# Optimization experiments

Measured on AMD Instinct MI355X. Metric: run time of the kernel, lower is better.

The kernel has to match this reference:

```python
import jax, jax.numpy as jnp
import numpy as np

B, C_IN, C_OUT, H, W = 16, 192, 192, 128, 128
K_EXPERTS, LATENT_DIM = 8, 64


def setup_inputs() -> dict:
    key = jax.random.key(0)
    ks = jax.random.split(key, 6)
    s = lambda fan: np.float32(1.0 / np.sqrt(fan))
    return {
        "x": jax.random.normal(ks[0], (B, C_IN, H, W), jnp.float32),
        "latent": jax.random.normal(ks[1], (B, LATENT_DIM), jnp.float32),
        # DyConv2d: K expert 3x3 kernels + biases, attention FC from latent
        "expert_w": jax.random.normal(ks[2], (K_EXPERTS, C_OUT, C_IN, 3, 3), jnp.float32) * s(C_IN * 9),
        "expert_b": jnp.zeros((K_EXPERTS, C_OUT), jnp.float32),
        "attn_w": jax.random.normal(ks[3], (K_EXPERTS, LATENT_DIM), jnp.float32) * s(LATENT_DIM),
        "attn_b": jnp.zeros((K_EXPERTS,), jnp.float32),
        # static conv2 (3x3) weights
        "conv2_w": jax.random.normal(ks[4], (C_OUT, C_OUT, 3, 3), jnp.float32) * s(C_OUT * 9),
        "conv2_b": jnp.zeros((C_OUT,), jnp.float32),
    }


def _conv3x3(x, w, b):
    # x: [N,C,H,W], w: [O,I,3,3] -> [N,O,H,W]
    y = jax.lax.conv_general_dilated(
        x, w, window_strides=(1, 1), padding=((1, 1), (1, 1)),
        dimension_numbers=("NCHW", "OIHW", "NCHW"))
    return y + b[None, :, None, None]


def reference(x, latent, expert_w, expert_b, attn_w, attn_b, conv2_w, conv2_b):
    identity = x  # stride=1, in_ch==out_ch -> adaptor is None
    # ---- DyConv2d: latent -> expert attention -> per-sample kernel ----
    attn = jax.nn.softmax(latent @ attn_w.T + attn_b, axis=-1)        # [B,K]
    w_dyn = jnp.einsum("bk,koihw->boihw", attn, expert_w)            # [B,O,I,3,3]
    b_dyn = attn @ expert_b                                          # [B,O]
    # per-sample conv, vectorized over batch
    out = jax.vmap(lambda xi, wi, bi: _conv3x3(xi[None], wi, bi)[0])(x, w_dyn, b_dyn)
    out = jax.nn.silu(out)
    # ---- static conv3x3 ----
    out = _conv3x3(out, conv2_w, conv2_b)
    out = jax.nn.silu(out)
    return out + identity
```

## Files before the change

### kernel.cpp

```cpp
#include <hip/hip_runtime.h>
#include <stdint.h>
#include <stddef.h>

typedef __bf16 bf16;
typedef bf16 bf16x8 __attribute__((ext_vector_type(8)));
typedef bf16 bf16x4 __attribute__((ext_vector_type(4)));
typedef float f32x4 __attribute__((ext_vector_type(4)));

#define B_   16
#define CI   192
#define CO   192
#define H_   128
#define W_   128
#define KE   8
#define LD   64
#define KTOT 1728
#define HP   130
#define HPHP (HP*HP)
#define NPX  (H_*W_)
#define NT   54

__device__ __forceinline__ void gll16(const void* g, void* l) {
  __builtin_amdgcn_global_load_lds(
      (const __attribute__((address_space(1))) unsigned int*)g,
      (__attribute__((address_space(3))) unsigned int*)l, 16, 0, 0);
}

__device__ __forceinline__ float silu_f(float x) {
  return x / (1.f + __expf(-x));
}

__global__ void k_attn(const float* __restrict__ latent, const float* __restrict__ attn_w,
                       const float* __restrict__ attn_b, float* __restrict__ attn) {
  int t = threadIdx.x;
  int b = t >> 3, k = t & 7;
  float s = attn_b[k];
  for (int d = 0; d < LD; ++d) s += latent[b*LD + d] * attn_w[k*LD + d];
  float m = s;
  for (int off = 4; off; off >>= 1) m = fmaxf(m, __shfl_xor(m, off, 8));
  float e = __expf(s - m);
  float sum = e;
  for (int off = 4; off; off >>= 1) sum += __shfl_xor(sum, off, 8);
  attn[t] = e / sum;
}

__global__ void k_bdyn(const float* __restrict__ attn, const float* __restrict__ expert_b,
                       float* __restrict__ bdyn) {
  int j = blockIdx.x * 256 + threadIdx.x;
  if (j >= B_ * CO) return;
  int b = j / CO, o = j - b * CO;
  float s = 0.f;
  #pragma unroll
  for (int e = 0; e < KE; ++e) s += attn[b*KE + e] * expert_b[e*CO + o];
  bdyn[j] = s;
}

__global__ void k_wdyn(const float* __restrict__ expert_w, const float* __restrict__ attn,
                       bf16* __restrict__ w_re) {
  int o = blockIdx.x;
  int chunk = o >> 4, row = o & 15, c = (row >> 1) & 3;
  __shared__ float ew[KE][KTOT];
  __shared__ float al[B_][KE];
  for (int e = 0; e < KE; ++e)
    for (int j = threadIdx.x; j < KTOT; j += 256)
      ew[e][j] = expert_w[((size_t)e*CO + o)*KTOT + j];
  if (threadIdx.x < B_*KE) al[threadIdx.x >> 3][threadIdx.x & 7] = attn[threadIdx.x];
  __syncthreads();
  for (int idx = threadIdx.x; idx < B_*KTOT; idx += 256) {
    int b = idx / KTOT, k = idx - b*KTOT;
    int kt = k >> 5, ks = (k >> 3) & 3, j = k & 7;
    int r = kt / 18, t2 = kt - r*18;
    int ibb = t2 / 3, s = t2 - ibb*3;
    int i = ibb*32 + ks*8 + j;
    float acc = 0.f;
    #pragma unroll
    for (int e = 0; e < KE; ++e) acc += al[b][e] * ew[e][i*9 + r*3 + s];
    int slot = row*4 + (ks ^ c);
    w_re[((((size_t)b*NT + kt)*12 + chunk)*64 + slot)*8 + j] = (bf16)acc;
  }
}

__global__ void k_w2re(const float* __restrict__ conv2_w, bf16* __restrict__ w2_re) {
  int o = blockIdx.x;
  int chunk = o >> 4, row = o & 15, c = (row >> 1) & 3;
  __shared__ float cw[KTOT];
  for (int j = threadIdx.x; j < KTOT; j += 256) cw[j] = conv2_w[(size_t)o*KTOT + j];
  __syncthreads();
  for (int k = threadIdx.x; k < KTOT; k += 256) {
    int kt = k >> 5, ks = (k >> 3) & 3, j = k & 7;
    int r = kt / 18, t2 = kt - r*18;
    int ibb = t2 / 3, s = t2 - ibb*3;
    int i = ibb*32 + ks*8 + j;
    int slot = row*4 + (ks ^ c);
    w2_re[(((size_t)kt*12 + chunk)*64 + slot)*8 + j] = (bf16)cw[i*9 + r*3 + s];
  }
}

__global__ void k_xpack(const float* __restrict__ x, bf16* __restrict__ xpack) {
  int h2 = blockIdx.x, ib = blockIdx.y, b = blockIdx.z;
  size_t rowbase = (((size_t)b*24 + ib)*HP + h2)*HP;
  int t = threadIdx.x;
  if (h2 == 0 || h2 == HP-1) {
    uint4 z = make_uint4(0,0,0,0);
    for (int w = t; w < HP; w += 128) *(uint4*)(xpack + (rowbase + w)*8) = z;
    return;
  }
  __shared__ float tt[8][128];
  int h = h2 - 1;
  #pragma unroll
  for (int ii = 0; ii < 8; ++ii)
    tt[ii][t] = x[(((size_t)b*CI + ib*8 + ii)*H_ + h)*W_ + t];
  __syncthreads();
  bf16x8 v;
  #pragma unroll
  for (int ii = 0; ii < 8; ++ii) v[ii] = (bf16)tt[ii][t];
  *(bf16x8*)(xpack + (rowbase + t + 1)*8) = v;
  if (t == 0) {
    uint4 z = make_uint4(0,0,0,0);
    *(uint4*)(xpack + rowbase*8) = z;
    *(uint4*)(xpack + (rowbase + HP-1)*8) = z;
  }
}

__global__ void k_midborder(bf16* __restrict__ midpack) {
  int bi = blockIdx.x;
  size_t base = (size_t)bi * HPHP;
  uint4 z = make_uint4(0,0,0,0);
  for (int j = threadIdx.x; j < 516; j += 256) {
    int h2, w2;
    if (j < 130)      { h2 = 0;       w2 = j; }
    else if (j < 260) { h2 = 129;     w2 = j - 130; }
    else if (j < 388) { h2 = j - 259; w2 = 0; }
    else              { h2 = j - 387; w2 = 129; }
    *(uint4*)(midpack + (base + (size_t)h2*HP + w2)*8) = z;
  }
}

template<int MODE>
__global__ __launch_bounds__(256, 2)
void k_conv(const bf16* __restrict__ wre, const bf16* __restrict__ inpack,
            const float* __restrict__ bias_g, const bf16* __restrict__ respack,
            bf16* __restrict__ outpack, float* __restrict__ outp) {
  const int tid  = threadIdx.x;
  const int lane = tid & 63;
  const int wv   = tid >> 6;
  const int wm   = wv >> 1;
  const int wn   = wv & 1;
  const int l15  = lane & 15, l4 = lane >> 4;

  const int bid  = blockIdx.x;
  const int n    = (bid & 7) * 128 + (bid >> 3);
  const int b    = n >> 6;
  const int tile = n & 63;
  const int p0   = tile * 256;
  const int h0   = tile * 2;

  __shared__ __align__(16) bf16 Alds[3][12*512];
  __shared__ __align__(16) bf16 Blds[2][4*2560];
  __shared__ float bias_lds[CO];

  if (tid < CO) bias_lds[tid] = (MODE == 0) ? bias_g[b*CO + tid] : bias_g[tid];

  const size_t wbase = (MODE == 0) ? ((size_t)b*CO*KTOT) : 0;

  const bf16* aS = wre + wbase + (size_t)wv*512 + lane*8;
  const bf16* bbase = inpack + (((size_t)b*24 + wv)*HPHP + (size_t)h0*HP)*8 + lane*8;
  int ibm = 0; ptrdiff_t boffEl = 0;

  auto stageA = [&](bf16* dbuf) {
    bf16* d = dbuf + wv*512;
    gll16(aS,        d);
    gll16(aS + 2048, d + 2048);
    gll16(aS + 4096, d + 4096);
    aS += 6144;
  };
  auto stageB = [&](bf16* dbuf) {
    const bf16* src = bbase + boffEl;
    bf16* d = dbuf + wv*2560;
    gll16(src,        d);
    gll16(src +  512, d +  512);
    gll16(src + 1024, d + 1024);
    gll16(src + 1536, d + 1536);
    gll16(src + 1568, d + 1568);
    if (++ibm == 6) { ibm = 0; boffEl += (ptrdiff_t)(HP - 20*HPHP)*8; }
    else boffEl += (ptrdiff_t)4*HPHP*8;
  };

  f32x4 acc[6][8];
  #pragma unroll
  for (int mf = 0; mf < 6; ++mf)
    #pragma unroll
    for (int nf = 0; nf < 8; ++nf)
      #pragma unroll
      for (int jj = 0; jj < 4; ++jj) acc[mf][nf][jj] = 0.f;

  const int sw = l15*4 + (l4 ^ ((l15 >> 1) & 3));
  const int bvb = l4*2560 + (wn*130 + l15)*8;

  stageA(Alds[0]);
  stageA(Alds[1]);
  stageB(Blds[0]);

  bf16* Bcur = (bf16*)Blds[0];
  bf16* Bnxt = (bf16*)Blds[1];

  for (int m = 0; m < 18; ++m) {
    #pragma unroll
    for (int s = 0; s < 3; ++s) {
      if (s == 2) {
        if (m == 17) asm volatile("s_waitcnt vmcnt(0)" ::: "memory");
        else         asm volatile("s_waitcnt vmcnt(8)" ::: "memory");
      } else {
        asm volatile("s_waitcnt vmcnt(3)" ::: "memory");
      }
      __builtin_amdgcn_s_barrier();

      const bf16* A = Alds[s];
      const bf16* bp = Bcur + bvb + s*8;

      bf16x8 af0 = *(const bf16x8*)(A + (wm*6 + 0)*512 + sw*8);
      bf16x8 af1 = *(const bf16x8*)(A + (wm*6 + 1)*512 + sw*8);
      bf16x8 af2 = *(const bf16x8*)(A + (wm*6 + 2)*512 + sw*8);
      bf16x8 af3 = *(const bf16x8*)(A + (wm*6 + 3)*512 + sw*8);
      bf16x8 af4 = *(const bf16x8*)(A + (wm*6 + 4)*512 + sw*8);
      bf16x8 af5 = *(const bf16x8*)(A + (wm*6 + 5)*512 + sw*8);
      bf16x8 bv0 = *(const bf16x8*)(bp);
      bf16x8 bv1 = *(const bf16x8*)(bp + 128);
      bf16x8 bv2 = *(const bf16x8*)(bp + 256);
      bf16x8 bv3 = *(const bf16x8*)(bp + 384);

      if (3*m + s + 2 < NT) stageA(Alds[(s+2)%3]);

      __builtin_amdgcn_s_barrier();
      __builtin_amdgcn_s_setprio(1);
      acc[0][0] = __builtin_amdgcn_mfma_f32_16x16x32_bf16(af0, bv0, acc[0][0], 0, 0, 0);
      acc[1][0] = __builtin_amdgcn_mfma_f32_16x16x32_bf16(af1, bv0, acc[1][0], 0, 0, 0);
      acc[2][0] = __builtin_amdgcn_mfma_f32_16x16x32_bf16(af2, bv0, acc[2][0], 0, 0, 0);
      acc[3][0] = __builtin_amdgcn_mfma_f32_16x16x32_bf16(af3, bv0, acc[3][0], 0, 0, 0);
      acc[4][0] = __builtin_amdgcn_mfma_f32_16x16x32_bf16(af4, bv0, acc[4][0], 0, 0, 0);
      acc[5][0] = __builtin_amdgcn_mfma_f32_16x16x32_bf16(af5, bv0, acc[5][0], 0, 0, 0);
      acc[0][1] = __builtin_amdgcn_mfma_f32_16x16x32_bf16(af0, bv1, acc[0][1], 0, 0, 0);
      acc[1][1] = __builtin_amdgcn_mfma_f32_16x16x32_bf16(af1, bv1, acc[1][1], 0, 0, 0);
      acc[2][1] = __builtin_amdgcn_mfma_f32_16x16x32_bf16(af2, bv1, acc[2][1], 0, 0, 0);
      acc[3][1] = __builtin_amdgcn_mfma_f32_16x16x32_bf16(af3, bv1, acc[3][1], 0, 0, 0);
      acc[4][1] = __builtin_amdgcn_mfma_f32_16x16x32_bf16(af4, bv1, acc[4][1], 0, 0, 0);
      acc[5][1] = __builtin_amdgcn_mfma_f32_16x16x32_bf16(af5, bv1, acc[5][1], 0, 0, 0);
      acc[0][2] = __builtin_amdgcn_mfma_f32_16x16x32_bf16(af0, bv2, acc[0][2], 0, 0, 0);
      acc[1][2] = __builtin_amdgcn_mfma_f32_16x16x32_bf16(af1, bv2, acc[1][2], 0, 0, 0);
      acc[2][2] = __builtin_amdgcn_mfma_f32_16x16x32_bf16(af2, bv2, acc[2][2], 0, 0, 0);
      acc[3][2] = __builtin_amdgcn_mfma_f32_16x16x32_bf16(af3, bv2, acc[3][2], 0, 0, 0);
      acc[4][2] = __builtin_amdgcn_mfma_f32_16x16x32_bf16(af4, bv2, acc[4][2], 0, 0, 0);
      acc[5][2] = __builtin_amdgcn_mfma_f32_16x16x32_bf16(af5, bv2, acc[5][2], 0, 0, 0);
      acc[0][3] = __builtin_amdgcn_mfma_f32_16x16x32_bf16(af0, bv3, acc[0][3], 0, 0, 0);
      acc[1][3] = __builtin_amdgcn_mfma_f32_16x16x32_bf16(af1, bv3, acc[1][3], 0, 0, 0);
      acc[2][3] = __builtin_amdgcn_mfma_f32_16x16x32_bf16(af2, bv3, acc[2][3], 0, 0, 0);
      acc[3][3] = __builtin_amdgcn_mfma_f32_16x16x32_bf16(af3, bv3, acc[3][3], 0, 0, 0);
      acc[4][3] = __builtin_amdgcn_mfma_f32_16x16x32_bf16(af4, bv3, acc[4][3], 0, 0, 0);
      acc[5][3] = __builtin_amdgcn_mfma_f32_16x16x32_bf16(af5, bv3, acc[5][3], 0, 0, 0);
      __builtin_amdgcn_s_setprio(0);

      bf16x8 bv4 = *(const bf16x8*)(bp + 512);
      bf16x8 bv5 = *(const bf16x8*)(bp + 640);
      bf16x8 bv6 = *(const bf16x8*)(bp + 768);
      bf16x8 bv7 = *(const bf16x8*)(bp + 896);

      if (s == 1 && m < 17) stageB(Bnxt);

      __builtin_amdgcn_s_barrier();
      __builtin_amdgcn_s_setprio(1);
      acc[0][4] = __builtin_amdgcn_mfma_f32_16x16x32_bf16(af0, bv4, acc[0][4], 0, 0, 0);
      acc[1][4] = __builtin_amdgcn_mfma_f32_16x16x32_bf16(af1, bv4, acc[1][4], 0, 0, 0);
      acc[2][4] = __builtin_amdgcn_mfma_f32_16x16x32_bf16(af2, bv4, acc[2][4], 0, 0, 0);
      acc[3][4] = __builtin_amdgcn_mfma_f32_16x16x32_bf16(af3, bv4, acc[3][4], 0, 0, 0);
      acc[4][4] = __builtin_amdgcn_mfma_f32_16x16x32_bf16(af4, bv4, acc[4][4], 0, 0, 0);
      acc[5][4] = __builtin_amdgcn_mfma_f32_16x16x32_bf16(af5, bv4, acc[5][4], 0, 0, 0);
      acc[0][5] = __builtin_amdgcn_mfma_f32_16x16x32_bf16(af0, bv5, acc[0][5], 0, 0, 0);
      acc[1][5] = __builtin_amdgcn_mfma_f32_16x16x32_bf16(af1, bv5, acc[1][5], 0, 0, 0);
      acc[2][5] = __builtin_amdgcn_mfma_f32_16x16x32_bf16(af2, bv5, acc[2][5], 0, 0, 0);
      acc[3][5] = __builtin_amdgcn_mfma_f32_16x16x32_bf16(af3, bv5, acc[3][5], 0, 0, 0);
      acc[4][5] = __builtin_amdgcn_mfma_f32_16x16x32_bf16(af4, bv5, acc[4][5], 0, 0, 0);
      acc[5][5] = __builtin_amdgcn_mfma_f32_16x16x32_bf16(af5, bv5, acc[5][5], 0, 0, 0);
      acc[0][6] = __builtin_amdgcn_mfma_f32_16x16x32_bf16(af0, bv6, acc[0][6], 0, 0, 0);
      acc[1][6] = __builtin_amdgcn_mfma_f32_16x16x32_bf16(af1, bv6, acc[1][6], 0, 0, 0);
      acc[2][6] = __builtin_amdgcn_mfma_f32_16x16x32_bf16(af2, bv6, acc[2][6], 0, 0, 0);
      acc[3][6] = __builtin_amdgcn_mfma_f32_16x16x32_bf16(af3, bv6, acc[3][6], 0, 0, 0);
      acc[4][6] = __builtin_amdgcn_mfma_f32_16x16x32_bf16(af4, bv6, acc[4][6], 0, 0, 0);
      acc[5][6] = __builtin_amdgcn_mfma_f32_16x16x32_bf16(af5, bv6, acc[5][6], 0, 0, 0);
      acc[0][7] = __builtin_amdgcn_mfma_f32_16x16x32_bf16(af0, bv7, acc[0][7], 0, 0, 0);
      acc[1][7] = __builtin_amdgcn_mfma_f32_16x16x32_bf16(af1, bv7, acc[1][7], 0, 0, 0);
      acc[2][7] = __builtin_amdgcn_mfma_f32_16x16x32_bf16(af2, bv7, acc[2][7], 0, 0, 0);
      acc[3][7] = __builtin_amdgcn_mfma_f32_16x16x32_bf16(af3, bv7, acc[3][7], 0, 0, 0);
      acc[4][7] = __builtin_amdgcn_mfma_f32_16x16x32_bf16(af4, bv7, acc[4][7], 0, 0, 0);
      acc[5][7] = __builtin_amdgcn_mfma_f32_16x16x32_bf16(af5, bv7, acc[5][7], 0, 0, 0);
      __builtin_amdgcn_s_setprio(0);
    }
    { bf16* t = Bcur; Bcur = Bnxt; Bnxt = t; }
  }

  #pragma unroll
  for (int mf = 0; mf < 6; ++mf) {
    int ob = wm*96 + mf*16 + l4*4;
    #pragma unroll
    for (int nf = 0; nf < 8; ++nf) {
      int pl = wn*128 + nf*16 + l15;
      int p  = p0 + pl;
      f32x4 v = acc[mf][nf];
      int h = p >> 7, w = p & 127;
      size_t basep = (((size_t)b*24 + (ob >> 3))*HP + (h + 1))*HP + (w + 1);
      if (MODE == 0) {
        bf16x4 pk;
        #pragma unroll
        for (int jj = 0; jj < 4; ++jj) {
          float xv = v[jj] + bias_lds[ob + jj];
          pk[jj] = (bf16)silu_f(xv);
        }
        *(bf16x4*)(outpack + basep*8 + (ob & 7)) = pk;
      } else {
        bf16x4 rr = *(const bf16x4*)(respack + basep*8 + (ob & 7));
        #pragma unroll
        for (int jj = 0; jj < 4; ++jj) {
          float xv = silu_f(v[jj] + bias_lds[ob + jj]);
          size_t idx = ((size_t)b*CO + ob + jj)*NPX + p;
          outp[idx] = xv + (float)rr[jj];
        }
      }
    }
  }
}

extern "C" void kernel_launch(void* const* d_in, const int* in_sizes, int n_in,
                              void* d_out, int out_size, void* d_ws, size_t ws_size,
                              hipStream_t stream) {
  const float* x        = (const float*)d_in[0];
  const float* latent   = (const float*)d_in[1];
  const float* expert_w = (const float*)d_in[2];
  const float* expert_b = (const float*)d_in[3];
  const float* attn_w   = (const float*)d_in[4];
  const float* attn_b   = (const float*)d_in[5];
  const float* conv2_w  = (const float*)d_in[6];
  const float* conv2_b  = (const float*)d_in[7];
  float* outp = (float*)d_out;

  char* base = (char*)d_ws;
  size_t off = 0;
  float* attn = (float*)(base + off); off += 4096;
  float* bdyn = (float*)(base + off); off += 16384;
  bf16* w_re  = (bf16*)(base + off);  off += (size_t)B_*CO*KTOT*2;
  bf16* w2_re = (bf16*)(base + off);  off += (size_t)CO*KTOT*2;
  bf16* xpack = (bf16*)(base + off);  off += (size_t)B_*24*HPHP*8*2;
  bf16* midpack = (bf16*)(base + off); off += (size_t)B_*24*HPHP*8*2;
  (void)ws_size; (void)in_sizes; (void)n_in; (void)out_size;

  k_attn<<<dim3(1), dim3(128), 0, stream>>>(latent, attn_w, attn_b, attn);
  k_bdyn<<<dim3(12), dim3(256), 0, stream>>>(attn, expert_b, bdyn);
  k_wdyn<<<dim3(CO), dim3(256), 0, stream>>>(expert_w, attn, w_re);
  k_w2re<<<dim3(CO), dim3(256), 0, stream>>>(conv2_w, w2_re);
  k_xpack<<<dim3(130, 24, 16), dim3(128), 0, stream>>>(x, xpack);
  k_midborder<<<dim3(B_*24), dim3(256), 0, stream>>>(midpack);
  k_conv<0><<<dim3(1024), dim3(256), 0, stream>>>(w_re, xpack, bdyn, xpack, midpack, outp);
  k_conv<1><<<dim3(1024), dim3(256), 0, stream>>>(w2_re, midpack, conv2_b, xpack, midpack, outp);
}
```

Before: 483.5 us.

## Load conv weight fragments directly from global into registers, dropping A LDS staging

Removes the triple-buffered LDS staging of the weight (A) operand. Each wave now reads its six weight fragments straight from global memory into registers at every k-step. The B tile pitch shrinks from 2560 to 2080 elements, and the per-substep barriers and manual vmcnt waits are collapsed into one __syncthreads per outer iteration. This cuts LDS footprint, LDS traffic and barrier count, which could also allow more resident blocks. The cost is that weight loads are issued right before the MFMAs with no prefetch, so global/L2 latency may be exposed every step. Correctness relies on __syncthreads draining the outstanding global-to-LDS B loads.

```diff
diff --git a/kernel.cpp b/kernel.cpp
--- a/kernel.cpp
+++ b/kernel.cpp
@@ -155,28 +155,17 @@
   const int p0   = tile * 256;
   const int h0   = tile * 2;
 
-  __shared__ __align__(16) bf16 Alds[3][12*512];
-  __shared__ __align__(16) bf16 Blds[2][4*2560];
+  __shared__ __align__(16) bf16 Blds[2][4*2080];
   __shared__ float bias_lds[CO];
 
-  if (tid < CO) bias_lds[tid] = (MODE == 0) ? bias_g[b*CO + tid] : bias_g[tid];
-
   const size_t wbase = (MODE == 0) ? ((size_t)b*CO*KTOT) : 0;
 
-  const bf16* aS = wre + wbase + (size_t)wv*512 + lane*8;
   const bf16* bbase = inpack + (((size_t)b*24 + wv)*HPHP + (size_t)h0*HP)*8 + lane*8;
   int ibm = 0; ptrdiff_t boffEl = 0;
 
-  auto stageA = [&](bf16* dbuf) {
-    bf16* d = dbuf + wv*512;
-    gll16(aS,        d);
-    gll16(aS + 2048, d + 2048);
-    gll16(aS + 4096, d + 4096);
-    aS += 6144;
-  };
   auto stageB = [&](bf16* dbuf) {
     const bf16* src = bbase + boffEl;
-    bf16* d = dbuf + wv*2560;
+    bf16* d = dbuf + wv*2080;
     gll16(src,        d);
     gll16(src +  512, d +  512);
     gll16(src + 1024, d + 1024);
@@ -186,6 +175,13 @@
     else boffEl += (ptrdiff_t)4*HPHP*8;
   };
 
+  stageB((bf16*)Blds[0]);
+
+  if (tid < CO) bias_lds[tid] = (MODE == 0) ? bias_g[b*CO + tid] : bias_g[tid];
+
+  const int sw = l15*4 + (l4 ^ ((l15 >> 1) & 3));
+  const bf16* aptr = wre + wbase + (size_t)(wm*6)*512 + (size_t)sw*8;
+
   f32x4 acc[6][8];
   #pragma unroll
   for (int mf = 0; mf < 6; ++mf)
@@ -194,106 +190,87 @@
       #pragma unroll
       for (int jj = 0; jj < 4; ++jj) acc[mf][nf][jj] = 0.f;
 
-  const int sw = l15*4 + (l4 ^ ((l15 >> 1) & 3));
-  const int bvb = l4*2560 + (wn*130 + l15)*8;
-
-  stageA(Alds[0]);
-  stageA(Alds[1]);
-  stageB(Blds[0]);
+  const int bvb = l4*2080 + (wn*130 + l15)*8;
 
   bf16* Bcur = (bf16*)Blds[0];
   bf16* Bnxt = (bf16*)Blds[1];
 
+  auto micro = [&](const bf16* Bc, int s, bool dostage, bf16* stagebuf) {
+    bf16x8 af0 = *(const bf16x8*)(aptr);
+    bf16x8 af1 = *(const bf16x8*)(aptr +  512);
+    bf16x8 af2 = *(const bf16x8*)(aptr + 1024);
+    bf16x8 af3 = *(const bf16x8*)(aptr + 1536);
+    bf16x8 af4 = *(const bf16x8*)(aptr + 2048);
+    bf16x8 af5 = *(const bf16x8*)(aptr + 2560);
+    aptr += 6144;
+    if (dostage) stageB(stagebuf);
+    const bf16* bp = Bc + bvb + s*8;
+    bf16x8 bv0 = *(const bf16x8*)(bp);
+    bf16x8 bv1 = *(const bf16x8*)(bp + 128);
+    bf16x8 bv2 = *(const bf16x8*)(bp + 256);
+    bf16x8 bv3 = *(const bf16x8*)(bp + 384);
+    bf16x8 bv4 = *(const bf16x8*)(bp + 512);
+    bf16x8 bv5 = *(const bf16x8*)(bp + 640);
+    bf16x8 bv6 = *(const bf16x8*)(bp + 768);
+    bf16x8 bv7 = *(const bf16x8*)(bp + 896);
+    __builtin_amdgcn_s_setprio(1);
+    acc[0][0] = __builtin_amdgcn_mfma_f32_16x16x32_bf16(af0, bv0, acc[0][0], 0, 0, 0);
+    acc[1][0] = __builtin_amdgcn_mfma_f32_16x16x32_bf16(af1, bv0, acc[1][0], 0, 0, 0);
+    acc[2][0] = __builtin_amdgcn_mfma_f32_16x16x32_bf16(af2, bv0, acc[2][0], 0, 0, 0);
+    acc[3][0] = __builtin_amdgcn_mfma_f32_16x16x32_bf16(af3, bv0, acc[3][0], 0, 0, 0);
+    acc[4][0] = __builtin_amdgcn_mfma_f32_16x16x32_bf16(af4, bv0, acc[4][0], 0, 0, 0);
+    acc[5][0] = __builtin_amdgcn_mfma_f32_16x16x32_bf16(af5, bv0, acc[5][0], 0, 0, 0);
+    acc[0][1] = __builtin_amdgcn_mfma_f32_16x16x32_bf16(af0, bv1, acc[0][1], 0, 0, 0);
+    acc[1][1] = __builtin_amdgcn_mfma_f32_16x16x32_bf16(af1, bv1, acc[1][1], 0, 0, 0);
+    acc[2][1] = __builtin_amdgcn_mfma_f32_16x16x32_bf16(af2, bv1, acc[2][1], 0, 0, 0);
+    acc[3][1] = __builtin_amdgcn_mfma_f32_16x16x32_bf16(af3, bv1, acc[3][1], 0, 0, 0);
+    acc[4][1] = __builtin_amdgcn_mfma_f32_16x16x32_bf16(af4, bv1, acc[4][1], 0, 0, 0);
+    acc[5][1] = __builtin_amdgcn_mfma_f32_16x16x32_bf16(af5, bv1, acc[5][1], 0, 0, 0);
+    acc[0][2] = __builtin_amdgcn_mfma_f32_16x16x32_bf16(af0, bv2, acc[0][2], 0, 0, 0);
+    acc[1][2] = __builtin_amdgcn_mfma_f32_16x16x32_bf16(af1, bv2, acc[1][2], 0, 0, 0);
+    acc[2][2] = __builtin_amdgcn_mfma_f32_16x16x32_bf16(af2, bv2, acc[2][2], 0, 0, 0);
+    acc[3][2] = __builtin_amdgcn_mfma_f32_16x16x32_bf16(af3, bv2, acc[3][2], 0, 0, 0);
+    acc[4][2] = __builtin_amdgcn_mfma_f32_16x16x32_bf16(af4, bv2, acc[4][2], 0, 0, 0);
+    acc[5][2] = __builtin_amdgcn_mfma_f32_16x16x32_bf16(af5, bv2, acc[5][2], 0, 0, 0);
+    acc[0][3] = __builtin_amdgcn_mfma_f32_16x16x32_bf16(af0, bv3, acc[0][3], 0, 0, 0);
+    acc[1][3] = __builtin_amdgcn_mfma_f32_16x16x32_bf16(af1, bv3, acc[1][3], 0, 0, 0);
+    acc[2][3] = __builtin_amdgcn_mfma_f32_16x16x32_bf16(af2, bv3, acc[2][3], 0, 0, 0);
+    acc[3][3] = __builtin_amdgcn_mfma_f32_16x16x32_bf16(af3, bv3, acc[3][3], 0, 0, 0);
+    acc[4][3] = __builtin_amdgcn_mfma_f32_16x16x32_bf16(af4, bv3, acc[4][3], 0, 0, 0);
+    acc[5][3] = __builtin_amdgcn_mfma_f32_16x16x32_bf16(af5, bv3, acc[5][3], 0, 0, 0);
+    acc[0][4] = __builtin_amdgcn_mfma_f32_16x16x32_bf16(af0, bv4, acc[0][4], 0, 0, 0);
+    acc[1][4] = __builtin_amdgcn_mfma_f32_16x16x32_bf16(af1, bv4, acc[1][4], 0, 0, 0);
+    acc[2][4] = __builtin_amdgcn_mfma_f32_16x16x32_bf16(af2, bv4, acc[2][4], 0, 0, 0);
+    acc[3][4] = __builtin_amdgcn_mfma_f32_16x16x32_bf16(af3, bv4, acc[3][4], 0, 0, 0);
+    acc[4][4] = __builtin_amdgcn_mfma_f32_16x16x32_bf16(af4, bv4, acc[4][4], 0, 0, 0);
+    acc[5][4] = __builtin_amdgcn_mfma_f32_16x16x32_bf16(af5, bv4, acc[5][4], 0, 0, 0);
+    acc[0][5] = __builtin_amdgcn_mfma_f32_16x16x32_bf16(af0, bv5, acc[0][5], 0, 0, 0);
+    acc[1][5] = __builtin_amdgcn_mfma_f32_16x16x32_bf16(af1, bv5, acc[1][5], 0, 0, 0);
+    acc[2][5] = __builtin_amdgcn_mfma_f32_16x16x32_bf16(af2, bv5, acc[2][5], 0, 0, 0);
+    acc[3][5] = __builtin_amdgcn_mfma_f32_16x16x32_bf16(af3, bv5, acc[3][5], 0, 0, 0);
+    acc[4][5] = __builtin_amdgcn_mfma_f32_16x16x32_bf16(af4, bv5, acc[4][5], 0, 0, 0);
+    acc[5][5] = __builtin_amdgcn_mfma_f32_16x16x32_bf16(af5, bv5, acc[5][5], 0, 0, 0);
+    acc[0][6] = __builtin_amdgcn_mfma_f32_16x16x32_bf16(af0, bv6, acc[0][6], 0, 0, 0);
+    acc[1][6] = __builtin_amdgcn_mfma_f32_16x16x32_bf16(af1, bv6, acc[1][6], 0, 0, 0);
+    acc[2][6] = __builtin_amdgcn_mfma_f32_16x16x32_bf16(af2, bv6, acc[2][6], 0, 0, 0);
+    acc[3][6] = __builtin_amdgcn_mfma_f32_16x16x32_bf16(af3, bv6, acc[3][6], 0, 0, 0);
+    acc[4][6] = __builtin_amdgcn_mfma_f32_16x16x32_bf16(af4, bv6, acc[4][6], 0, 0, 0);
+    acc[5][6] = __builtin_amdgcn_mfma_f32_16x16x32_bf16(af5, bv6, acc[5][6], 0, 0, 0);
+    acc[0][7] = __builtin_amdgcn_mfma_f32_16x16x32_bf16(af0, bv7, acc[0][7], 0, 0, 0);
+    acc[1][7] = __builtin_amdgcn_mfma_f32_16x16x32_bf16(af1, bv7, acc[1][7], 0, 0, 0);
+    acc[2][7] = __builtin_amdgcn_mfma_f32_16x16x32_bf16(af2, bv7, acc[2][7], 0, 0, 0);
+    acc[3][7] = __builtin_amdgcn_mfma_f32_16x16x32_bf16(af3, bv7, acc[3][7], 0, 0, 0);
+    acc[4][7] = __builtin_amdgcn_mfma_f32_16x16x32_bf16(af4, bv7, acc[4][7], 0, 0, 0);
+    acc[5][7] = __builtin_amdgcn_mfma_f32_16x16x32_bf16(af5, bv7, acc[5][7], 0, 0, 0);
+    __builtin_amdgcn_s_setprio(0);
+    __builtin_amdgcn_sched_barrier(0);
+  };
+
   for (int m = 0; m < 18; ++m) {
-    #pragma unroll
-    for (int s = 0; s < 3; ++s) {
-      if (s == 2) {
-        if (m == 17) asm volatile("s_waitcnt vmcnt(0)" ::: "memory");
-        else         asm volatile("s_waitcnt vmcnt(8)" ::: "memory");
-      } else {
-        asm volatile("s_waitcnt vmcnt(3)" ::: "memory");
-      }
-      __builtin_amdgcn_s_barrier();
-
-      const bf16* A = Alds[s];
-      const bf16* bp = Bcur + bvb + s*8;
-
-      bf16x8 af0 = *(const bf16x8*)(A + (wm*6 + 0)*512 + sw*8);
-      bf16x8 af1 = *(const bf16x8*)(A + (wm*6 + 1)*512 + sw*8);
-      bf16x8 af2 = *(const bf16x8*)(A + (wm*6 + 2)*512 + sw*8);
-      bf16x8 af3 = *(const bf16x8*)(A + (wm*6 + 3)*512 + sw*8);
-      bf16x8 af4 = *(const bf16x8*)(A + (wm*6 + 4)*512 + sw*8);
-      bf16x8 af5 = *(const bf16x8*)(A + (wm*6 + 5)*512 + sw*8);
-      bf16x8 bv0 = *(const bf16x8*)(bp);
-      bf16x8 bv1 = *(const bf16x8*)(bp + 128);
-      bf16x8 bv2 = *(const bf16x8*)(bp + 256);
-      bf16x8 bv3 = *(const bf16x8*)(bp + 384);
-
-      if (3*m + s + 2 < NT) stageA(Alds[(s+2)%3]);
-
-      __builtin_amdgcn_s_barrier();
-      __builtin_amdgcn_s_setprio(1);
-      acc[0][0] = __builtin_amdgcn_mfma_f32_16x16x32_bf16(af0, bv0, acc[0][0], 0, 0, 0);
-      acc[1][0] = __builtin_amdgcn_mfma_f32_16x16x32_bf16(af1, bv0, acc[1][0], 0, 0, 0);
-      acc[2][0] = __builtin_amdgcn_mfma_f32_16x16x32_bf16(af2, bv0, acc[2][0], 0, 0, 0);
-      acc[3][0] = __builtin_amdgcn_mfma_f32_16x16x32_bf16(af3, bv0, acc[3][0], 0, 0, 0);
-      acc[4][0] = __builtin_amdgcn_mfma_f32_16x16x32_bf16(af4, bv0, acc[4][0], 0, 0, 0);
-      acc[5][0] = __builtin_amdgcn_mfma_f32_16x16x32_bf16(af5, bv0, acc[5][0], 0, 0, 0);
-      acc[0][1] = __builtin_amdgcn_mfma_f32_16x16x32_bf16(af0, bv1, acc[0][1], 0, 0, 0);
-      acc[1][1] = __builtin_amdgcn_mfma_f32_16x16x32_bf16(af1, bv1, acc[1][1], 0, 0, 0);
-      acc[2][1] = __builtin_amdgcn_mfma_f32_16x16x32_bf16(af2, bv1, acc[2][1], 0, 0, 0);
-      acc[3][1] = __builtin_amdgcn_mfma_f32_16x16x32_bf16(af3, bv1, acc[3][1], 0, 0, 0);
-      acc[4][1] = __builtin_amdgcn_mfma_f32_16x16x32_bf16(af4, bv1, acc[4][1], 0, 0, 0);
-      acc[5][1] = __builtin_amdgcn_mfma_f32_16x16x32_bf16(af5, bv1, acc[5][1], 0, 0, 0);
-      acc[0][2] = __builtin_amdgcn_mfma_f32_16x16x32_bf16(af0, bv2, acc[0][2], 0, 0, 0);
-      acc[1][2] = __builtin_amdgcn_mfma_f32_16x16x32_bf16(af1, bv2, acc[1][2], 0, 0, 0);
-      acc[2][2] = __builtin_amdgcn_mfma_f32_16x16x32_bf16(af2, bv2, acc[2][2], 0, 0, 0);
-      acc[3][2] = __builtin_amdgcn_mfma_f32_16x16x32_bf16(af3, bv2, acc[3][2], 0, 0, 0);
-      acc[4][2] = __builtin_amdgcn_mfma_f32_16x16x32_bf16(af4, bv2, acc[4][2], 0, 0, 0);
-      acc[5][2] = __builtin_amdgcn_mfma_f32_16x16x32_bf16(af5, bv2, acc[5][2], 0, 0, 0);
-      acc[0][3] = __builtin_amdgcn_mfma_f32_16x16x32_bf16(af0, bv3, acc[0][3], 0, 0, 0);
-      acc[1][3] = __builtin_amdgcn_mfma_f32_16x16x32_bf16(af1, bv3, acc[1][3], 0, 0, 0);
-      acc[2][3] = __builtin_amdgcn_mfma_f32_16x16x32_bf16(af2, bv3, acc[2][3], 0, 0, 0);
-      acc[3][3] = __builtin_amdgcn_mfma_f32_16x16x32_bf16(af3, bv3, acc[3][3], 0, 0, 0);
-      acc[4][3] = __builtin_amdgcn_mfma_f32_16x16x32_bf16(af4, bv3, acc[4][3], 0, 0, 0);
-      acc[5][3] = __builtin_amdgcn_mfma_f32_16x16x32_bf16(af5, bv3, acc[5][3], 0, 0, 0);
-      __builtin_amdgcn_s_setprio(0);
-
-      bf16x8 bv4 = *(const bf16x8*)(bp + 512);
-      bf16x8 bv5 = *(const bf16x8*)(bp + 640);
-      bf16x8 bv6 = *(const bf16x8*)(bp + 768);
-      bf16x8 bv7 = *(const bf16x8*)(bp + 896);
-
-      if (s == 1 && m < 17) stageB(Bnxt);
-
-      __builtin_amdgcn_s_barrier();
-      __builtin_amdgcn_s_setprio(1);
-      acc[0][4] = __builtin_amdgcn_mfma_f32_16x16x32_bf16(af0, bv4, acc[0][4], 0, 0, 0);
-      acc[1][4] = __builtin_amdgcn_mfma_f32_16x16x32_bf16(af1, bv4, acc[1][4], 0, 0, 0);
-      acc[2][4] = __builtin_amdgcn_mfma_f32_16x16x32_bf16(af2, bv4, acc[2][4], 0, 0, 0);
-      acc[3][4] = __builtin_amdgcn_mfma_f32_16x16x32_bf16(af3, bv4, acc[3][4], 0, 0, 0);
-      acc[4][4] = __builtin_amdgcn_mfma_f32_16x16x32_bf16(af4, bv4, acc[4][4], 0, 0, 0);
-      acc[5][4] = __builtin_amdgcn_mfma_f32_16x16x32_bf16(af5, bv4, acc[5][4], 0, 0, 0);
-      acc[0][5] = __builtin_amdgcn_mfma_f32_16x16x32_bf16(af0, bv5, acc[0][5], 0, 0, 0);
-      acc[1][5] = __builtin_amdgcn_mfma_f32_16x16x32_bf16(af1, bv5, acc[1][5], 0, 0, 0);
-      acc[2][5] = __builtin_amdgcn_mfma_f32_16x16x32_bf16(af2, bv5, acc[2][5], 0, 0, 0);
-      acc[3][5] = __builtin_amdgcn_mfma_f32_16x16x32_bf16(af3, bv5, acc[3][5], 0, 0, 0);
-      acc[4][5] = __builtin_amdgcn_mfma_f32_16x16x32_bf16(af4, bv5, acc[4][5], 0, 0, 0);
-      acc[5][5] = __builtin_amdgcn_mfma_f32_16x16x32_bf16(af5, bv5, acc[5][5], 0, 0, 0);
-      acc[0][6] = __builtin_amdgcn_mfma_f32_16x16x32_bf16(af0, bv6, acc[0][6], 0, 0, 0);
-      acc[1][6] = __builtin_amdgcn_mfma_f32_16x16x32_bf16(af1, bv6, acc[1][6], 0, 0, 0);
-      acc[2][6] = __builtin_amdgcn_mfma_f32_16x16x32_bf16(af2, bv6, acc[2][6], 0, 0, 0);
-      acc[3][6] = __builtin_amdgcn_mfma_f32_16x16x32_bf16(af3, bv6, acc[3][6], 0, 0, 0);
-      acc[4][6] = __builtin_amdgcn_mfma_f32_16x16x32_bf16(af4, bv6, acc[4][6], 0, 0, 0);
-      acc[5][6] = __builtin_amdgcn_mfma_f32_16x16x32_bf16(af5, bv6, acc[5][6], 0, 0, 0);
-      acc[0][7] = __builtin_amdgcn_mfma_f32_16x16x32_bf16(af0, bv7, acc[0][7], 0, 0, 0);
-      acc[1][7] = __builtin_amdgcn_mfma_f32_16x16x32_bf16(af1, bv7, acc[1][7], 0, 0, 0);
-      acc[2][7] = __builtin_amdgcn_mfma_f32_16x16x32_bf16(af2, bv7, acc[2][7], 0, 0, 0);
-      acc[3][7] = __builtin_amdgcn_mfma_f32_16x16x32_bf16(af3, bv7, acc[3][7], 0, 0, 0);
-      acc[4][7] = __builtin_amdgcn_mfma_f32_16x16x32_bf16(af4, bv7, acc[4][7], 0, 0, 0);
-      acc[5][7] = __builtin_amdgcn_mfma_f32_16x16x32_bf16(af5, bv7, acc[5][7], 0, 0, 0);
-      __builtin_amdgcn_s_setprio(0);
-    }
+    __syncthreads();
+    micro(Bcur, 0, false, nullptr);
+    micro(Bcur, 1, false, nullptr);
+    micro(Bcur, 2, m < 17, Bnxt);
     { bf16* t = Bcur; Bcur = Bnxt; Bnxt = t; }
   }
 
```

New measurement: 543.4 us. 12.4% more time.
